# Kernel tuning notes

Measured on AMD Instinct MI355X. Metric: run time of the kernel, lower is better.

Reference implementation:

```python
import jax, jax.numpy as jnp
import numpy as np

POS_THR = 0.7
NEG_THR = 0.3
SAMPLE_BATCH = 256
POS_FRAC = 0.5
B, K, H, W, G = 8, 9, 64, 64, 128
A = K * H * W  # 36864 total anchors


def _make_boxes(key, lead_shape, img=1024.0, wmin=16.0, wmax=256.0):
    k1, k2 = jax.random.split(key)
    ctr = jax.random.uniform(k1, lead_shape + (2,), minval=0.0, maxval=img)
    wh = jax.random.uniform(k2, lead_shape + (2,), minval=wmin, maxval=wmax)
    return jnp.concatenate([ctr - wh / 2, ctr + wh / 2], axis=-1)


def setup_inputs() -> dict:
    key = jax.random.key(0)
    k1, k2, k3, k4 = jax.random.split(key, 4)
    return {
        "cls_logits": jax.random.normal(k1, (B, K, H, W), dtype=jnp.float32),
        "bbox_pred": jax.random.normal(k2, (B, 4 * K, H, W), dtype=jnp.float32) * 0.1,
        "anchors": _make_boxes(k3, (A,)),
        "gt_boxes": _make_boxes(k4, (B, G)),
    }


def _compute_iou(a, g):
    # a: [A,4], g: [G,4] -> [A,G]
    lt = jnp.maximum(a[:, None, :2], g[None, :, :2])
    rb = jnp.minimum(a[:, None, 2:], g[None, :, 2:])
    wh = jnp.clip(rb - lt, 0.0)
    inter = wh[..., 0] * wh[..., 1]
    area_a = (a[:, 2] - a[:, 0]) * (a[:, 3] - a[:, 1])
    area_g = (g[:, 2] - g[:, 0]) * (g[:, 3] - g[:, 1])
    return inter / (area_a[:, None] + area_g[None, :] - inter + 1e-6)


def _encode(anchors, gt):
    aw = anchors[:, 2] - anchors[:, 0]
    ah = anchors[:, 3] - anchors[:, 1]
    acx = (anchors[:, 0] + anchors[:, 2]) / 2
    acy = (anchors[:, 1] + anchors[:, 3]) / 2
    gw = gt[:, 2] - gt[:, 0]
    gh = gt[:, 3] - gt[:, 1]
    gcx = (gt[:, 0] + gt[:, 2]) / 2
    gcy = (gt[:, 1] + gt[:, 3]) / 2
    return jnp.stack([(gcx - acx) / aw, (gcy - acy) / ah,
                      jnp.log(gw / aw), jnp.log(gh / ah)], axis=1)


def _subsample(labels, mask, target, key):
    # deterministic-key analog of torch.randperm subsampling: random priorities,
    # keep the `target` highest-priority anchors of the masked class.
    score = jnp.where(mask, jax.random.uniform(key, labels.shape), -1.0)
    order = jnp.argsort(-score)
    rank = jnp.zeros_like(order).at[order].set(jnp.arange(order.shape[0]))
    keep = mask & (rank < target)
    return jnp.where(mask & ~keep, -1, labels)


def _per_image(cls_i, box_i, anchors, gt, key):
    iou = _compute_iou(anchors, gt)                      # [A,G]
    max_iou = iou.max(axis=1)
    matched_gt_idx = iou.argmax(axis=1)
    labels = jnp.where(max_iou < NEG_THR, 0, -1)
    labels = jnp.where(max_iou >= POS_THR, 1, labels)
    matched_anchor_idx = iou.argmax(axis=0)              # [G]
    labels = labels.at[matched_anchor_idx].set(1)        # force best anchor per gt
    bbox_targets = _encode(anchors, gt[matched_gt_idx])  # [A,4]

    k1, k2 = jax.random.split(key)
    pos_mask0 = labels == 1
    num_pos = pos_mask0.sum()
    target_pos = jnp.minimum(jnp.int32(SAMPLE_BATCH * POS_FRAC), num_pos)
    labels = _subsample(labels, pos_mask0, target_pos, k1)
    neg_mask0 = labels == 0
    num_neg = neg_mask0.sum()
    target_neg = jnp.minimum(SAMPLE_BATCH - target_pos, num_neg)
    labels = _subsample(labels, neg_mask0, target_neg, k2)

    valid = (labels >= 0).astype(cls_i.dtype)
    z = (labels == 1).astype(cls_i.dtype)
    # BCEWithLogits: softplus(x) - x*z
    bce = jax.nn.softplus(cls_i) - cls_i * z
    cls_loss = (bce * valid).sum() / jnp.maximum(valid.sum(), 1.0)

    pos = (labels == 1).astype(cls_i.dtype)
    d = box_i - bbox_targets
    ad = jnp.abs(d)
    sl1 = jnp.where(ad < 1.0, 0.5 * d * d, ad - 0.5)     # SmoothL1, beta=1
    bbox_loss = (sl1 * pos[:, None]).sum() / jnp.maximum(4.0 * pos.sum(), 1.0)
    return cls_loss, bbox_loss


def reference(cls_logits, bbox_pred, anchors, gt_boxes):
    b = cls_logits.shape[0]
    cls = cls_logits.transpose(0, 2, 3, 1).reshape(b, -1)          # [B,A]
    box = bbox_pred.transpose(0, 2, 3, 1).reshape(b, -1, 4)        # [B,A,4]
    keys = jax.random.split(jax.random.key(42), b)
    cls_l, box_l = jax.vmap(_per_image, in_axes=(0, 0, None, 0, 0))(
        cls, box, anchors, gt_boxes, keys)
    cls_loss = cls_l.mean()
    bbox_loss = box_l.mean()
    return jnp.stack([cls_loss, bbox_loss, cls_loss + bbox_loss])
```

## Files before the change

### kernel.cpp

```cpp
#include <hip/hip_runtime.h>
#include <stdint.h>
#include <limits.h>

#define PARTITIONABLE 1

#define B_ 8
#define K_ 9
#define H_ 64
#define W_ 64
#define G_ 128
#define A_ 36864
#define HALF_A 18432
#define QUART_A 9216
#define NBUCK 8192
#define CAP 1024
#define NBEST 4096
#define NLAB  1152

struct KeyParams { uint32_t k[B_][4]; };

__host__ __device__ static inline uint32_t rotl32(uint32_t x, int r) {
  return (x << r) | (x >> (32 - r));
}

__host__ __device__ static inline void tf2x32(uint32_t k0, uint32_t k1,
                                              uint32_t x0, uint32_t x1,
                                              uint32_t& o0, uint32_t& o1) {
  uint32_t ks2 = k0 ^ k1 ^ 0x1BD11BDAu;
  x0 += k0; x1 += k1;
#define TF_R(r) { x0 += x1; x1 = rotl32(x1, r); x1 ^= x0; }
  TF_R(13) TF_R(15) TF_R(26) TF_R(6)
  x0 += k1;  x1 += ks2 + 1u;
  TF_R(17) TF_R(29) TF_R(16) TF_R(24)
  x0 += ks2; x1 += k0 + 2u;
  TF_R(13) TF_R(15) TF_R(26) TF_R(6)
  x0 += k0;  x1 += k1 + 3u;
  TF_R(17) TF_R(29) TF_R(16) TF_R(24)
  x0 += k1;  x1 += ks2 + 4u;
  TF_R(13) TF_R(15) TF_R(26) TF_R(6)
  x0 += ks2; x1 += k0 + 5u;
#undef TF_R
  o0 = x0; o1 = x1;
}

__device__ static inline uint32_t anchor_vbits(uint32_t k0, uint32_t k1, int a) {
  uint32_t o0, o1;
#if PARTITIONABLE
  tf2x32(k0, k1, 0u, (uint32_t)a, o0, o1);
  return (o0 ^ o1) >> 9;
#else
  if (a < HALF_A) { tf2x32(k0, k1, (uint32_t)a, (uint32_t)(a + HALF_A), o0, o1); return o0 >> 9; }
  else            { tf2x32(k0, k1, (uint32_t)(a - HALF_A), (uint32_t)a, o0, o1); return o1 >> 9; }
#endif
}

__device__ static inline float area_of(float x0, float y0, float x1, float y1) {
#pragma clang fp contract(off)
  return (x1 - x0) * (y1 - y0);
}

__device__ static inline float iou_fn(float a0, float a1, float a2, float a3,
                                      float g0, float g1, float g2, float g3) {
#pragma clang fp contract(off)
  float ltx = fmaxf(a0, g0), lty = fmaxf(a1, g1);
  float rbx = fminf(a2, g2), rby = fminf(a3, g3);
  float w = rbx - ltx; w = (w < 0.f) ? 0.f : w;
  float h = rby - lty; h = (h < 0.f) ? 0.f : h;
  float inter  = w * h;
  float area_a = (a2 - a0) * (a3 - a1);
  float area_g = (g2 - g0) * (g3 - g1);
  return inter / (area_a + area_g - inter + 1e-6f);
}

__device__ static inline float iou_pre_a(float a0, float a1, float a2, float a3,
                                         float area_a,
                                         float g0, float g1, float g2, float g3) {
#pragma clang fp contract(off)
  float ltx = fmaxf(a0, g0), lty = fmaxf(a1, g1);
  float rbx = fminf(a2, g2), rby = fminf(a3, g3);
  float w = rbx - ltx; w = (w < 0.f) ? 0.f : w;
  float h = rby - lty; h = (h < 0.f) ? 0.f : h;
  float inter  = w * h;
  float area_g = (g2 - g0) * (g3 - g1);
  return inter / (area_a + area_g - inter + 1e-6f);
}

__device__ static inline void encode4(float4 an, float4 gg, float* tt) {
#pragma clang fp contract(off)
  float aw  = an.z - an.x,            ah  = an.w - an.y;
  float acx = (an.x + an.z) * 0.5f,   acy = (an.y + an.w) * 0.5f;
  float gw  = gg.z - gg.x,            gh  = gg.w - gg.y;
  float gcx = (gg.x + gg.z) * 0.5f,   gcy = (gg.y + gg.w) * 0.5f;
  tt[0] = (gcx - acx) / aw;
  tt[1] = (gcy - acy) / ah;
  tt[2] = logf(gw / aw);
  tt[3] = logf(gh / ah);
}

__device__ static inline int block_reduce_int(int v, int* sh) {
  int t = threadIdx.x;
  sh[t] = v; __syncthreads();
  for (int s = 128; s > 0; s >>= 1) { if (t < s) sh[t] += sh[t + s]; __syncthreads(); }
  int r = sh[0]; __syncthreads();
  return r;
}
__device__ static inline float block_reduce_float(float v, float* sh) {
  int t = threadIdx.x;
  sh[t] = v; __syncthreads();
  for (int s = 128; s > 0; s >>= 1) { if (t < s) sh[t] += sh[t + s]; __syncthreads(); }
  float r = sh[0]; __syncthreads();
  return r;
}

__device__ static inline unsigned long long pack_vi(float v, int a) {
  return ((unsigned long long)__float_as_uint(v) << 32) | (uint32_t)(~(uint32_t)a);
}

__global__ __launch_bounds__(256) void fused_iou_k(const float* __restrict__ anchors,
                                                   const float* __restrict__ gtb,
                                                   int* __restrict__ labels,
                                                   int* __restrict__ mgt,
                                                   uint32_t* __restrict__ vpos,
                                                   uint32_t* __restrict__ vneg,
                                                   int* __restrict__ ghist,
                                                   int* __restrict__ counts,
                                                   unsigned long long* __restrict__ gmax,
                                                   KeyParams kp) {
  __shared__ unsigned long long sp[256];
  __shared__ float4 gts[G_];
  __shared__ int red[256];
  const int bid = blockIdx.x;
  const int t = threadIdx.x;

  if (bid < NBEST) {
    const int bg = bid & 1023;
    const int base = (bid >> 10) * QUART_A;
    float4 gg = ((const float4*)gtb)[bg];
    float v0 = -1.f, v1 = -1.f, v2 = -1.f, v3 = -1.f;
    int   i0 = 0,    i1 = 0,    i2 = 0,    i3 = 0;
    for (int a = base + t; a < base + QUART_A; a += 1024) {
      float4 an0 = ((const float4*)anchors)[a];
      float4 an1 = ((const float4*)anchors)[a + 256];
      float4 an2 = ((const float4*)anchors)[a + 512];
      float4 an3 = ((const float4*)anchors)[a + 768];
      float w0 = iou_fn(an0.x, an0.y, an0.z, an0.w, gg.x, gg.y, gg.z, gg.w);
      float w1 = iou_fn(an1.x, an1.y, an1.z, an1.w, gg.x, gg.y, gg.z, gg.w);
      float w2 = iou_fn(an2.x, an2.y, an2.z, an2.w, gg.x, gg.y, gg.z, gg.w);
      float w3 = iou_fn(an3.x, an3.y, an3.z, an3.w, gg.x, gg.y, gg.z, gg.w);
      if (w0 > v0) { v0 = w0; i0 = a; }
      if (w1 > v1) { v1 = w1; i1 = a + 256; }
      if (w2 > v2) { v2 = w2; i2 = a + 512; }
      if (w3 > v3) { v3 = w3; i3 = a + 768; }
    }
    unsigned long long p = pack_vi(v0, i0);
    unsigned long long q = pack_vi(v1, i1); if (q > p) p = q;
    q = pack_vi(v2, i2); if (q > p) p = q;
    q = pack_vi(v3, i3); if (q > p) p = q;
    sp[t] = p; __syncthreads();
    for (int s = 128; s > 0; s >>= 1) {
      if (t < s) { if (sp[t + s] > sp[t]) sp[t] = sp[t + s]; }
      __syncthreads();
    }
    if (t == 0) atomicMax(&gmax[bg], sp[0]);
    return;
  }

  const int r = bid - NBEST;
  const int b = r / (A_ / 256);
  const int xb = r % (A_ / 256);
  for (int i = t; i < G_; i += 256) gts[i] = ((const float4*)gtb)[b * G_ + i];
  __syncthreads();
  const int a = xb * 256 + t;
  float4 an = ((const float4*)anchors)[a];
  float area_a = area_of(an.x, an.y, an.z, an.w);
  float bv = -1.f; int bi = 0;
#pragma unroll 4
  for (int g = 0; g < G_; g++) {
    float4 gg = gts[g];
    float v = iou_pre_a(an.x, an.y, an.z, an.w, area_a,
                        gg.x, gg.y, gg.z, gg.w);
    if (v > bv) { bv = v; bi = g; }
  }
  int lb = (bv < 0.3f) ? 0 : ((bv >= 0.7f) ? 1 : -1);
  size_t idx = (size_t)b * A_ + a;
  uint32_t vp = anchor_vbits(kp.k[b][0], kp.k[b][1], a);
  uint32_t vn = anchor_vbits(kp.k[b][2], kp.k[b][3], a);
  labels[idx] = lb;
  mgt[idx]    = bi;
  vpos[idx]   = vp;
  vneg[idx]   = vn;
  if (lb == 1)      atomicAdd(&ghist[(b * 2 + 0) * NBUCK + (vp >> 10)], 1);
  else if (lb == 0) atomicAdd(&ghist[(b * 2 + 1) * NBUCK + (vn >> 10)], 1);
  int packed = (lb == 1 ? 1 : 0) | ((lb == 0 ? 1 : 0) << 16);
  int rr = block_reduce_int(packed, red);
  if (t == 0) {
    atomicAdd(&counts[b * 2 + 0], rr & 0xFFFF);
    atomicAdd(&counts[b * 2 + 1], rr >> 16);
  }
}

__global__ void force_k(const unsigned long long* __restrict__ gmax,
                        int* __restrict__ labels,
                        const uint32_t* __restrict__ vpos,
                        const uint32_t* __restrict__ vneg,
                        int* __restrict__ ghist,
                        int* __restrict__ counts) {
  int tg = blockIdx.x * 256 + threadIdx.x;
  int b = tg / G_;
  int a = (int)(~(uint32_t)(gmax[tg] & 0xFFFFFFFFull));
  size_t idx = (size_t)b * A_ + a;
  int old = atomicExch(&labels[idx], 1);
  if (old != 1) {
    atomicAdd(&counts[b * 2 + 0], 1);
    atomicAdd(&ghist[(b * 2 + 0) * NBUCK + (vpos[idx] >> 10)], 1);
    if (old == 0) {
      atomicSub(&counts[b * 2 + 1], 1);
      atomicSub(&ghist[(b * 2 + 1) * NBUCK + (vneg[idx] >> 10)], 1);
    }
  }
}

__global__ __launch_bounds__(256) void cutoff_k(const int* __restrict__ ghist,
                                                const int* __restrict__ counts,
                                                int* __restrict__ cbR,
                                                int* __restrict__ targets) {
  const int row = blockIdx.x;
  const int b = row >> 1, c = row & 1;
  const int t = threadIdx.x;
  __shared__ int seg[256];
  int npos = counts[b * 2 + 0], nneg = counts[b * 2 + 1];
  int tp = npos < 128 ? npos : 128;
  int tn = 256 - tp; if (nneg < tn) tn = nneg;
  const int target = (c == 0) ? tp : tn;
  const int* hist = ghist + (size_t)row * NBUCK;
  { int s = 0; const int base = t * 32;
    for (int i = 0; i < 32; i++) s += hist[base + i];
    seg[t] = s; }
  __syncthreads();
  if (t == 0) {
    int cb = INT_MAX, R = 0;
    if (target > 0) {
      int cum = 0, si = -1;
      for (int i = 255; i >= 0; i--) { if (cum + seg[i] >= target) { si = i; break; } cum += seg[i]; }
      for (int j = si * 32 + 31; j >= si * 32; j--) {
        if (cum + hist[j] >= target) { cb = j; R = target - cum; break; }
        cum += hist[j];
      }
    }
    cbR[row * 2 + 0] = cb;
    cbR[row * 2 + 1] = R;
    targets[row] = target;
  }
}

__global__ __launch_bounds__(256) void cand_k(const int* __restrict__ labels,
                                              const uint32_t* __restrict__ vpos,
                                              const uint32_t* __restrict__ vneg,
                                              const int* __restrict__ cbR,
                                              int* __restrict__ ccnt,
                                              uint32_t* __restrict__ cvv,
                                              int* __restrict__ cii) {
  const int b = blockIdx.y;
  const int a = blockIdx.x * 256 + threadIdx.x;
  size_t idx = (size_t)b * A_ + a;
  int lb = labels[idx];
  if (lb < 0) return;
  int c = (lb == 1) ? 0 : 1;
  int row = b * 2 + c;
  uint32_t v = (c == 0 ? vpos : vneg)[idx];
  if ((int)(v >> 10) == cbR[row * 2]) {
    int p = atomicAdd(&ccnt[row], 1);
    if (p < CAP) { cvv[row * CAP + p] = v; cii[row * CAP + p] = a; }
  }
}

__global__ __launch_bounds__(256) void loss_k(const float* __restrict__ anchors,
                                              const float* __restrict__ gtb,
                                              const float* __restrict__ cls,
                                              const float* __restrict__ boxp,
                                              const int* __restrict__ labels,
                                              const int* __restrict__ mgt,
                                              const uint32_t* __restrict__ vpos,
                                              const uint32_t* __restrict__ vneg,
                                              const int* __restrict__ cbR,
                                              const int* __restrict__ ccnt,
                                              const uint32_t* __restrict__ cvv,
                                              const int* __restrict__ cii,
                                              float* __restrict__ bsums) {
  const int b = blockIdx.y;
  const int a = blockIdx.x * 256 + threadIdx.x;
  const int t = threadIdx.x;
  __shared__ float redf[256];
  float sb = 0.f, ss = 0.f;
  size_t idx = (size_t)b * A_ + a;
  int lb = labels[idx];
  if (lb >= 0) {
    int c = (lb == 1) ? 0 : 1;
    int row = b * 2 + c;
    uint32_t v = (c == 0 ? vpos : vneg)[idx];
    int bucket = (int)(v >> 10);
    int cb = cbR[row * 2];
    bool kept = bucket > cb;
    if (!kept && bucket == cb) {
      int c2 = ccnt[row]; if (c2 > CAP) c2 = CAP;
      int R = cbR[row * 2 + 1];
      int r = 0;
      for (int j = 0; j < c2; j++) {
        uint32_t vj = cvv[row * CAP + j]; int ij = cii[row * CAP + j];
        if (vj > v || (vj == v && ij < a)) r++;
      }
      kept = (r < R);
    }
    if (kept) {
      int kk = a % K_; int hw = a / K_; int hh = hw / W_; int wx = hw % W_;
      float x  = cls[(((size_t)b * K_ + kk) * H_ + hh) * W_ + wx];
      float sp = fmaxf(x, 0.f) + log1pf(expf(-fabsf(x)));
      sb = (lb == 1) ? (sp - x) : sp;
      if (lb == 1) {
        float4 an = ((const float4*)anchors)[a];
        int    mg = mgt[idx];
        float4 gg = ((const float4*)gtb)[b * G_ + mg];
        float tt[4]; encode4(an, gg, tt);
        for (int cc = 0; cc < 4; cc++) {
          float p = boxp[(((size_t)b * (4 * K_) + (4 * kk + cc)) * H_ + hh) * W_ + wx];
          float d = p - tt[cc];
          float ad = fabsf(d);
          ss += (ad < 1.f) ? (0.5f * d * d) : (ad - 0.5f);
        }
      }
    }
  }
  float sbT = block_reduce_float(sb, redf);
  float ssT = block_reduce_float(ss, redf);
  if (t == 0) {
    if (sbT != 0.f) atomicAdd(&bsums[b * 2 + 0], sbT);
    if (ssT != 0.f) atomicAdd(&bsums[b * 2 + 1], ssT);
  }
}

__global__ void final_k(const float* __restrict__ bsums, const int* __restrict__ targets,
                        float* __restrict__ out) {
  if (threadIdx.x == 0 && blockIdx.x == 0) {
    float cl = 0.f, bl = 0.f;
    for (int b = 0; b < B_; b++) {
      int tp = targets[b * 2 + 0], tn = targets[b * 2 + 1];
      cl += bsums[b * 2 + 0] / fmaxf((float)(tp + tn), 1.f);
      bl += bsums[b * 2 + 1] / fmaxf(4.f * (float)tp, 1.f);
    }
    cl *= 0.125f; bl *= 0.125f;
    out[0] = cl; out[1] = bl; out[2] = cl + bl;
  }
}

static void compute_keys(KeyParams& kp) {
  const uint32_t r0 = 0u, r1 = 42u;
#if PARTITIONABLE
  for (int b = 0; b < B_; b++) {
    uint32_t kb0, kb1;
    tf2x32(r0, r1, 0u, (uint32_t)b, kb0, kb1);
    uint32_t a0, a1, c0, c1;
    tf2x32(kb0, kb1, 0u, 0u, a0, a1);
    tf2x32(kb0, kb1, 0u, 1u, c0, c1);
    kp.k[b][0] = a0; kp.k[b][1] = a1; kp.k[b][2] = c0; kp.k[b][3] = c1;
  }
#else
  uint32_t o0[8], o1[8], flat[16];
  for (int i = 0; i < 8; i++) tf2x32(r0, r1, (uint32_t)i, (uint32_t)(8 + i), o0[i], o1[i]);
  for (int i = 0; i < 8; i++) { flat[i] = o0[i]; flat[8 + i] = o1[i]; }
  for (int b = 0; b < B_; b++) {
    uint32_t kb0 = flat[2 * b], kb1 = flat[2 * b + 1];
    uint32_t a0, b0, a1, b1;
    tf2x32(kb0, kb1, 0u, 2u, a0, b0);
    tf2x32(kb0, kb1, 1u, 3u, a1, b1);
    kp.k[b][0] = a0; kp.k[b][1] = a1; kp.k[b][2] = b0; kp.k[b][3] = b1;
  }
#endif
}

extern "C" void kernel_launch(void* const* d_in, const int* in_sizes, int n_in,
                              void* d_out, int out_size, void* d_ws, size_t ws_size,
                              hipStream_t stream) {
  const float* cls     = (const float*)d_in[0];
  const float* boxp    = (const float*)d_in[1];
  const float* anchors = (const float*)d_in[2];
  const float* gtb     = (const float*)d_in[3];
  float* out = (float*)d_out;

  uint8_t* w = (uint8_t*)d_ws;
  unsigned long long* gmax = (unsigned long long*)w;
  int*      ghist   = (int*)(w + 8192);
  int*      counts  = (int*)(w + 532480);
  int*      ccnt    = counts + 16;
  float*    bsums   = (float*)(ccnt + 16);
  int*      labels  = (int*)(w + 532672);
  int*      mgt     = labels + (size_t)B_ * A_;
  uint32_t* vpos    = (uint32_t*)(mgt + (size_t)B_ * A_);
  uint32_t* vneg    = vpos + (size_t)B_ * A_;
  int*      cbR     = (int*)(vneg + (size_t)B_ * A_);
  int*      targets = cbR + 32;
  uint32_t* cvv     = (uint32_t*)(targets + 16);
  int*      cii     = (int*)(cvv + 16 * CAP);

  KeyParams kp;
  compute_keys(kp);

  (void)hipMemsetAsync(w, 0, 532672, stream);
  fused_iou_k<<<NBEST + NLAB, 256, 0, stream>>>(anchors, gtb, labels, mgt,
                                                vpos, vneg, ghist, counts, gmax, kp);
  force_k<<<(B_ * G_) / 256, 256, 0, stream>>>(gmax, labels, vpos, vneg, ghist, counts);
  cutoff_k<<<16, 256, 0, stream>>>(ghist, counts, cbR, targets);
  cand_k<<<dim3(A_ / 256, B_), 256, 0, stream>>>(labels, vpos, vneg, cbR, ccnt, cvv, cii);
  loss_k<<<dim3(A_ / 256, B_), 256, 0, stream>>>(anchors, gtb, cls, boxp, labels, mgt,
                                                 vpos, vneg, cbR, ccnt, cvv, cii, bsums);
  final_k<<<1, 64, 0, stream>>>(bsums, targets, out);
}
```

Baseline: 174.8 us.

## Fold forced-positive pass into cutoff kernel and finalize loss in last block

Merges the force-positive and cutoff kernels into one mid kernel. It copies each histogram row into shared memory, applies the forced-positive flips locally and records the flipped anchors in a small list, so labels are no longer rewritten. The candidate and loss kernels read that list to treat flipped anchors as positive. The final reduction moves into the last loss block, found through an atomic done counter, which removes two launches. In exchange, each thread scans a flip list of up to 128 entries, and the code relies on a threadfence and last-block pattern to be correct.

```diff
diff --git a/kernel.cpp b/kernel.cpp
--- a/kernel.cpp
+++ b/kernel.cpp
@@ -16,6 +16,7 @@
 #define CAP 1024
 #define NBEST 4096
 #define NLAB  1152
+#define NLOSS 1152
 
 struct KeyParams { uint32_t k[B_][4]; };
 
@@ -199,42 +200,55 @@
   }
 }
 
-__global__ void force_k(const unsigned long long* __restrict__ gmax,
-                        int* __restrict__ labels,
-                        const uint32_t* __restrict__ vpos,
-                        const uint32_t* __restrict__ vneg,
-                        int* __restrict__ ghist,
-                        int* __restrict__ counts) {
-  int tg = blockIdx.x * 256 + threadIdx.x;
-  int b = tg / G_;
-  int a = (int)(~(uint32_t)(gmax[tg] & 0xFFFFFFFFull));
-  size_t idx = (size_t)b * A_ + a;
-  int old = atomicExch(&labels[idx], 1);
-  if (old != 1) {
-    atomicAdd(&counts[b * 2 + 0], 1);
-    atomicAdd(&ghist[(b * 2 + 0) * NBUCK + (vpos[idx] >> 10)], 1);
-    if (old == 0) {
-      atomicSub(&counts[b * 2 + 1], 1);
-      atomicSub(&ghist[(b * 2 + 1) * NBUCK + (vneg[idx] >> 10)], 1);
-    }
-  }
-}
-
-__global__ __launch_bounds__(256) void cutoff_k(const int* __restrict__ ghist,
-                                                const int* __restrict__ counts,
-                                                int* __restrict__ cbR,
-                                                int* __restrict__ targets) {
+__global__ __launch_bounds__(256) void mid_k(const unsigned long long* __restrict__ gmax,
+                                             const int* __restrict__ labels,
+                                             const uint32_t* __restrict__ vpos,
+                                             const uint32_t* __restrict__ vneg,
+                                             const int* __restrict__ ghist,
+                                             const int* __restrict__ counts,
+                                             int* __restrict__ cbR,
+                                             int* __restrict__ targets,
+                                             int* __restrict__ flist,
+                                             int* __restrict__ fcnt) {
   const int row = blockIdx.x;
   const int b = row >> 1, c = row & 1;
   const int t = threadIdx.x;
+  __shared__ int hl[NBUCK];
+  __shared__ int fa[G_];
+  __shared__ int red[256];
   __shared__ int seg[256];
-  int npos = counts[b * 2 + 0], nneg = counts[b * 2 + 1];
+  __shared__ int fcount;
+
+  for (int i = t; i < NBUCK; i += 256) hl[i] = ghist[(size_t)row * NBUCK + i];
+  if (t < G_) fa[t] = (int)(~(uint32_t)(gmax[b * G_ + t] & 0xFFFFFFFFull));
+  if (t == 0) fcount = 0;
+  __syncthreads();
+
+  int flip = 0, wasneg = 0, mya = 0;
+  if (t < G_) {
+    mya = fa[t];
+    int uniq = 1;
+    for (int g = 0; g < t; g++) if (fa[g] == mya) { uniq = 0; break; }
+    if (uniq) {
+      int oldl = labels[(size_t)b * A_ + mya];
+      flip = (oldl != 1);
+      wasneg = (oldl == 0);
+    }
+  }
+  if (c == 0) { if (flip)   atomicAdd(&hl[vpos[(size_t)b * A_ + mya] >> 10], 1); }
+  else        { if (wasneg) atomicSub(&hl[vneg[(size_t)b * A_ + mya] >> 10], 1); }
+  if (c == 0 && flip) { int p = atomicAdd(&fcount, 1); flist[b * G_ + p] = mya; }
+
+  int dsum = block_reduce_int(flip | (wasneg << 16), red);
+  int npos = counts[b * 2 + 0] + (dsum & 0xFFFF);
+  int nneg = counts[b * 2 + 1] - (dsum >> 16);
   int tp = npos < 128 ? npos : 128;
   int tn = 256 - tp; if (nneg < tn) tn = nneg;
   const int target = (c == 0) ? tp : tn;
-  const int* hist = ghist + (size_t)row * NBUCK;
+  if (c == 0 && t == 0) fcnt[b] = fcount;
+
   { int s = 0; const int base = t * 32;
-    for (int i = 0; i < 32; i++) s += hist[base + i];
+    for (int i = 0; i < 32; i++) s += hl[base + i];
     seg[t] = s; }
   __syncthreads();
   if (t == 0) {
@@ -243,29 +257,47 @@
       int cum = 0, si = -1;
       for (int i = 255; i >= 0; i--) { if (cum + seg[i] >= target) { si = i; break; } cum += seg[i]; }
       for (int j = si * 32 + 31; j >= si * 32; j--) {
-        if (cum + hist[j] >= target) { cb = j; R = target - cum; break; }
-        cum += hist[j];
+        if (cum + hl[j] >= target) { cb = j; R = target - cum; break; }
+        cum += hl[j];
       }
     }
     cbR[row * 2 + 0] = cb;
     cbR[row * 2 + 1] = R;
     targets[row] = target;
   }
+}
+
+__device__ static inline bool is_pos_post(int lb, int a, const int* fl, int fn) {
+  if (lb == 1) return true;
+  for (int j = 0; j < fn; j++) if (fl[j] == a) return true;
+  return false;
 }
 
 __global__ __launch_bounds__(256) void cand_k(const int* __restrict__ labels,
                                               const uint32_t* __restrict__ vpos,
                                               const uint32_t* __restrict__ vneg,
                                               const int* __restrict__ cbR,
+                                              const int* __restrict__ flist,
+                                              const int* __restrict__ fcnt,
                                               int* __restrict__ ccnt,
                                               uint32_t* __restrict__ cvv,
                                               int* __restrict__ cii) {
   const int b = blockIdx.y;
-  const int a = blockIdx.x * 256 + threadIdx.x;
+  const int t = threadIdx.x;
+  __shared__ int fl[G_];
+  __shared__ int fn_s;
+  if (t == 0) fn_s = fcnt[b];
+  if (t < G_) fl[t] = flist[b * G_ + t];
+  __syncthreads();
+  const int fn = fn_s;
+  const int a = blockIdx.x * 256 + t;
   size_t idx = (size_t)b * A_ + a;
   int lb = labels[idx];
-  if (lb < 0) return;
-  int c = (lb == 1) ? 0 : 1;
+  bool pos = is_pos_post(lb, a, fl, fn);
+  int c;
+  if (pos) c = 0;
+  else if (lb == 0) c = 1;
+  else return;
   int row = b * 2 + c;
   uint32_t v = (c == 0 ? vpos : vneg)[idx];
   if ((int)(v >> 10) == cbR[row * 2]) {
@@ -286,16 +318,30 @@
                                               const int* __restrict__ ccnt,
                                               const uint32_t* __restrict__ cvv,
                                               const int* __restrict__ cii,
-                                              float* __restrict__ bsums) {
+                                              const int* __restrict__ flist,
+                                              const int* __restrict__ fcnt,
+                                              const int* __restrict__ targets,
+                                              float* __restrict__ bsums,
+                                              int* __restrict__ done,
+                                              float* __restrict__ out) {
   const int b = blockIdx.y;
-  const int a = blockIdx.x * 256 + threadIdx.x;
   const int t = threadIdx.x;
   __shared__ float redf[256];
+  __shared__ int fl[G_];
+  __shared__ int fn_s;
+  __shared__ int amlast;
+  if (t == 0) fn_s = fcnt[b];
+  if (t < G_) fl[t] = flist[b * G_ + t];
+  __syncthreads();
+  const int fn = fn_s;
+  const int a = blockIdx.x * 256 + t;
   float sb = 0.f, ss = 0.f;
   size_t idx = (size_t)b * A_ + a;
   int lb = labels[idx];
-  if (lb >= 0) {
-    int c = (lb == 1) ? 0 : 1;
+  bool pos = is_pos_post(lb, a, fl, fn);
+  bool valid = pos || (lb == 0);
+  if (valid) {
+    int c = pos ? 0 : 1;
     int row = b * 2 + c;
     uint32_t v = (c == 0 ? vpos : vneg)[idx];
     int bucket = (int)(v >> 10);
@@ -315,8 +361,8 @@
       int kk = a % K_; int hw = a / K_; int hh = hw / W_; int wx = hw % W_;
       float x  = cls[(((size_t)b * K_ + kk) * H_ + hh) * W_ + wx];
       float sp = fmaxf(x, 0.f) + log1pf(expf(-fabsf(x)));
-      sb = (lb == 1) ? (sp - x) : sp;
-      if (lb == 1) {
+      sb = pos ? (sp - x) : sp;
+      if (pos) {
         float4 an = ((const float4*)anchors)[a];
         int    mg = mgt[idx];
         float4 gg = ((const float4*)gtb)[b * G_ + mg];
@@ -335,17 +381,20 @@
   if (t == 0) {
     if (sbT != 0.f) atomicAdd(&bsums[b * 2 + 0], sbT);
     if (ssT != 0.f) atomicAdd(&bsums[b * 2 + 1], ssT);
-  }
-}
-
-__global__ void final_k(const float* __restrict__ bsums, const int* __restrict__ targets,
-                        float* __restrict__ out) {
-  if (threadIdx.x == 0 && blockIdx.x == 0) {
+    __threadfence();
+    int old = atomicAdd(done, 1);
+    amlast = (old == NLOSS - 1);
+  }
+  __syncthreads();
+  if (t == 0 && amlast) {
+    __threadfence();
     float cl = 0.f, bl = 0.f;
-    for (int b = 0; b < B_; b++) {
-      int tp = targets[b * 2 + 0], tn = targets[b * 2 + 1];
-      cl += bsums[b * 2 + 0] / fmaxf((float)(tp + tn), 1.f);
-      bl += bsums[b * 2 + 1] / fmaxf(4.f * (float)tp, 1.f);
+    for (int b2 = 0; b2 < B_; b2++) {
+      int tp = targets[b2 * 2 + 0], tn = targets[b2 * 2 + 1];
+      float s0 = atomicAdd(&bsums[b2 * 2 + 0], 0.0f);
+      float s1 = atomicAdd(&bsums[b2 * 2 + 1], 0.0f);
+      cl += s0 / fmaxf((float)(tp + tn), 1.f);
+      bl += s1 / fmaxf(4.f * (float)tp, 1.f);
     }
     cl *= 0.125f; bl *= 0.125f;
     out[0] = cl; out[1] = bl; out[2] = cl + bl;
@@ -392,7 +441,8 @@
   int*      counts  = (int*)(w + 532480);
   int*      ccnt    = counts + 16;
   float*    bsums   = (float*)(ccnt + 16);
-  int*      labels  = (int*)(w + 532672);
+  int*      done    = (int*)(bsums + 16);
+  int*      labels  = (int*)(w + 532736);
   int*      mgt     = labels + (size_t)B_ * A_;
   uint32_t* vpos    = (uint32_t*)(mgt + (size_t)B_ * A_);
   uint32_t* vneg    = vpos + (size_t)B_ * A_;
@@ -400,17 +450,20 @@
   int*      targets = cbR + 32;
   uint32_t* cvv     = (uint32_t*)(targets + 16);
   int*      cii     = (int*)(cvv + 16 * CAP);
+  int*      flist   = cii + 16 * CAP;
+  int*      fcnt    = flist + B_ * G_;
 
   KeyParams kp;
   compute_keys(kp);
 
-  (void)hipMemsetAsync(w, 0, 532672, stream);
+  (void)hipMemsetAsync(w, 0, 532736, stream);
   fused_iou_k<<<NBEST + NLAB, 256, 0, stream>>>(anchors, gtb, labels, mgt,
                                                 vpos, vneg, ghist, counts, gmax, kp);
-  force_k<<<(B_ * G_) / 256, 256, 0, stream>>>(gmax, labels, vpos, vneg, ghist, counts);
-  cutoff_k<<<16, 256, 0, stream>>>(ghist, counts, cbR, targets);
-  cand_k<<<dim3(A_ / 256, B_), 256, 0, stream>>>(labels, vpos, vneg, cbR, ccnt, cvv, cii);
+  mid_k<<<16, 256, 0, stream>>>(gmax, labels, vpos, vneg, ghist, counts,
+                                cbR, targets, flist, fcnt);
+  cand_k<<<dim3(A_ / 256, B_), 256, 0, stream>>>(labels, vpos, vneg, cbR,
+                                                 flist, fcnt, ccnt, cvv, cii);
   loss_k<<<dim3(A_ / 256, B_), 256, 0, stream>>>(anchors, gtb, cls, boxp, labels, mgt,
-                                                 vpos, vneg, cbR, ccnt, cvv, cii, bsums);
-  final_k<<<1, 64, 0, stream>>>(bsums, targets, out);
-}
+                                                 vpos, vneg, cbR, ccnt, cvv, cii,
+                                                 flist, fcnt, targets, bsums, done, out);
+}
```

Result: slower. 198.0 us (+13.2%).
